# Optimization experiments

Measured on AMD Instinct MI355X. Metric: run time of the kernel, lower is better.

Reference implementation:

```python
import jax, jax.numpy as jnp
import numpy as np

N_PATCHES = 7
HIDDEN = 256
HEADS = 8
BLOCKS = 4
OUT_D = 1000
BATCH = 256
C, H_IMG, W_IMG = 3, 224, 224
N_TOK = N_PATCHES ** 2 + 1  # 50 (CLS at node 0)
INPUT_D = C * (H_IMG // N_PATCHES) * (W_IMG // N_PATCHES)  # 3072
MLP_D = 4 * HIDDEN


def build_edge_index():
    # replicates get_squere_edge_index: 8-neighborhood grid (nodes shifted +1)
    # plus patch->CLS edges. Row 0 = source, row 1 = target (PyG convention).
    s, d = [], []
    for i in range(N_PATCHES):
        for j in range(N_PATCHES):
            a = i + j * N_PATCHES + 1
            for di, dj in [(-1, 0), (-1, -1), (0, -1), (1, -1), (1, 0), (1, 1), (0, 1), (-1, 1)]:
                ii, jj = i + di, j + dj
                if 0 <= ii < N_PATCHES and 0 <= jj < N_PATCHES:
                    s.append(a); d.append(ii + jj * N_PATCHES + 1)
    for i in range(N_PATCHES):
        for j in range(N_PATCHES):
            s.append(i + j * N_PATCHES + 1); d.append(0)
    return np.array([s, d], dtype=np.int64)


def pos_emb(S, d):
    i = jnp.arange(S, dtype=jnp.float32)[:, None]
    j = jnp.arange(d)
    jeff = (j // 2 * 2).astype(jnp.float32)
    ang = i / jnp.power(jnp.float32(10000.0), jeff / d)
    return jnp.where(j % 2 == 0, jnp.sin(ang), jnp.cos(ang))


def layer_norm(x, g, b):
    mu = x.mean(-1, keepdims=True)
    var = ((x - mu) ** 2).mean(-1, keepdims=True)
    return (x - mu) / jnp.sqrt(var + 1e-5) * g + b


def gat(x, src, dst, W, a_s, a_d, bias):
    # PyG GATConv: lin (no bias), per-head additive attention, LeakyReLU(0.2),
    # softmax over incoming edges per target, concat heads, + bias.
    B, N, _ = x.shape
    H, Dh = a_s.shape
    h = (x @ W).reshape(B, N, H, Dh)
    al_s = jnp.einsum('bnhd,hd->bnh', h, a_s)
    al_d = jnp.einsum('bnhd,hd->bnh', h, a_d)
    e = jax.nn.leaky_relu(al_s[:, src] + al_d[:, dst], 0.2)  # [B,E,H]
    seg_max = jax.vmap(lambda v: jax.ops.segment_max(v, dst, num_segments=N))
    seg_sum = jax.vmap(lambda v: jax.ops.segment_sum(v, dst, num_segments=N))
    m = jax.lax.stop_gradient(seg_max(e))
    ex = jnp.exp(e - m[:, dst])
    alpha = ex / (seg_sum(ex)[:, dst] + 1e-16)
    out = seg_sum(h[:, src] * alpha[..., None])  # [B,N,H,Dh]
    return out.reshape(B, N, H * Dh) + bias


def setup_inputs() -> dict:
    key = jax.random.key(0)
    ks = jax.random.split(key, 16)
    sc = 0.05
    L = BLOCKS
    inp = {
        'images': jax.random.normal(ks[0], (BATCH, C, H_IMG, W_IMG), jnp.float32),
        'edge_index': jnp.asarray(build_edge_index()),
        'Wmap': jax.random.normal(ks[1], (INPUT_D, HIDDEN), jnp.float32) * sc,
        'bmap': jax.random.normal(ks[2], (HIDDEN,), jnp.float32) * sc,
        'cls_tok': jax.random.uniform(ks[3], (1, HIDDEN), jnp.float32),
        'Wgat': jax.random.normal(ks[4], (L, HIDDEN, HIDDEN), jnp.float32) * sc,
        'att_src': jax.random.normal(ks[5], (L, HEADS, HIDDEN // HEADS), jnp.float32) * sc,
        'att_dst': jax.random.normal(ks[6], (L, HEADS, HIDDEN // HEADS), jnp.float32) * sc,
        'bgat': jax.random.normal(ks[7], (L, HIDDEN), jnp.float32) * sc,
        'ln1_g': jnp.ones((L, HIDDEN), jnp.float32),
        'ln1_b': jnp.zeros((L, HIDDEN), jnp.float32),
        'ln2_g': jnp.ones((L, HIDDEN), jnp.float32),
        'ln2_b': jnp.zeros((L, HIDDEN), jnp.float32),
        'W1': jax.random.normal(ks[8], (L, HIDDEN, MLP_D), jnp.float32) * sc,
        'b1': jax.random.normal(ks[9], (L, MLP_D), jnp.float32) * sc,
        'W2': jax.random.normal(ks[10], (L, MLP_D, HIDDEN), jnp.float32) * sc,
        'b2': jax.random.normal(ks[11], (L, HIDDEN), jnp.float32) * sc,
        'Wout': jax.random.normal(ks[12], (HIDDEN, OUT_D), jnp.float32) * sc,
        'bout': jax.random.normal(ks[13], (OUT_D,), jnp.float32) * sc,
    }
    return inp


def reference(images, edge_index, Wmap, bmap, cls_tok, Wgat, att_src, att_dst, bgat,
              ln1_g, ln1_b, ln2_g, ln2_b, W1, b1, W2, b2, Wout, bout):
    n, c, h, w = images.shape
    ps = h // N_PATCHES
    # vectorized patchify: [n, np^2, c*ps*ps] in (c, hh, ww) flatten order
    patches = images.reshape(n, c, N_PATCHES, ps, N_PATCHES, ps)
    patches = patches.transpose(0, 2, 4, 1, 3, 5).reshape(n, N_PATCHES ** 2, c * ps * ps)
    tok = patches @ Wmap + bmap
    tok = jnp.concatenate([jnp.broadcast_to(cls_tok, (n, 1, HIDDEN)), tok], axis=1)
    out = tok + pos_emb(N_TOK, HIDDEN)
    loops = jnp.arange(N_TOK)  # GATConv add_self_loops
    src = jnp.concatenate([edge_index[0], loops])
    dst = jnp.concatenate([edge_index[1], loops])
    for l in range(BLOCKS):
        out = out + gat(layer_norm(out, ln1_g[l], ln1_b[l]), src, dst,
                        Wgat[l], att_src[l], att_dst[l], bgat[l])
        h2 = layer_norm(out, ln2_g[l], ln2_b[l])
        out = out + (jax.nn.gelu(h2 @ W1[l] + b1[l], approximate=False) @ W2[l] + b2[l])
    return jax.nn.softmax(out[:, 0] @ Wout + bout, axis=-1)
```

## Files before the change

### kernel.cpp

```cpp
#include <hip/hip_runtime.h>
#include <hip/hip_bf16.h>

#define BATCH   256
#define NTOK    50
#define NPATCH  49
#define HID     256
#define HEADS   8
#define DH      32
#define NBLK    4
#define MLPD    1024
#define OUTD    1000
#define KPATCH  3072
#define MROWS   (BATCH*NTOK)
#define MPATCH  (BATCH*NPATCH)
#define MAXDEG  12

typedef __attribute__((ext_vector_type(4))) float  floatx4;
typedef __attribute__((ext_vector_type(8))) __bf16 bf16x8;
typedef __attribute__((ext_vector_type(4))) int    int4v;
typedef __attribute__((ext_vector_type(4))) short  short4v;

__device__ __forceinline__ bool tag_is_bf16(const unsigned short* tag) {
    return tag[0] == 0x3F80u;
}
__device__ __forceinline__ float ldf(const void* p, long i, bool bf) {
    return bf ? __bfloat162float(((const __hip_bfloat16*)p)[i])
              : ((const float*)p)[i];
}
__device__ __forceinline__ short bf16s(float x) {
    __hip_bfloat16 h = __float2bfloat16(x);
    return *(short*)&h;
}

__device__ __forceinline__ float fast_gelu(float u) {
    float s  = u * 0.70710678118654752f;
    float ax = fabsf(s);
    float t  = 1.f / (1.f + 0.3275911f * ax);
    float p  = fmaf(1.061405429f, t, -1.453152027f);
    p = fmaf(p, t, 1.421413741f);
    p = fmaf(p, t, -0.284496736f);
    p = fmaf(p, t, 0.254829592f);
    p *= t;
    float er = copysignf(1.f - p * __expf(-s * s), s);
    return 0.5f * u * (1.f + er);
}

#define OFF_BMAP 0
#define OFF_CLS  256
#define OFF_ASRC 512
#define OFF_ADST 1536
#define OFF_BGAT 2560
#define OFF_LN1G 3584
#define OFF_LN1B 4608
#define OFF_LN2G 5632
#define OFF_LN2B 6656
#define OFF_B1   7680
#define OFF_B2   11776
#define OFF_BOUT 12800
#define SP_TOTAL 13800

struct SmallSrc {
    const void *bmap, *cls, *asrc, *adst, *bgat, *ln1g, *ln1b, *ln2g, *ln2b, *b1, *b2, *bout;
};

__global__ void pack_params(SmallSrc s, const unsigned short* tag,
                            __hip_bfloat16* __restrict__ sp) {
    bool bf = tag_is_bf16(tag);
    int idx = blockIdx.x * 256 + threadIdx.x;
    if (idx >= SP_TOTAL) return;
    const void* src; long off;
    if      (idx < OFF_CLS)  { src = s.bmap; off = idx; }
    else if (idx < OFF_ASRC) { src = s.cls;  off = idx - OFF_CLS; }
    else if (idx < OFF_ADST) { src = s.asrc; off = idx - OFF_ASRC; }
    else if (idx < OFF_BGAT) { src = s.adst; off = idx - OFF_ADST; }
    else if (idx < OFF_LN1G) { src = s.bgat; off = idx - OFF_BGAT; }
    else if (idx < OFF_LN1B) { src = s.ln1g; off = idx - OFF_LN1G; }
    else if (idx < OFF_LN2G) { src = s.ln1b; off = idx - OFF_LN1B; }
    else if (idx < OFF_LN2B) { src = s.ln2g; off = idx - OFF_LN2G; }
    else if (idx < OFF_B1)   { src = s.ln2b; off = idx - OFF_LN2B; }
    else if (idx < OFF_B2)   { src = s.b1;   off = idx - OFF_B1; }
    else if (idx < OFF_BOUT) { src = s.b2;   off = idx - OFF_B2; }
    else                     { src = s.bout; off = idx - OFF_BOUT; }
    sp[idx] = __float2bfloat16(ldf(src, off, bf));
}

__global__ void prep_kernel(const int* __restrict__ ei, int E0,
                            float* __restrict__ adj, float* __restrict__ pe,
                            int* __restrict__ nbrI, float* __restrict__ nbrW,
                            int* __restrict__ deg) {
    int tid = threadIdx.x;
    if (blockIdx.x == 0) {
        for (int i = tid; i < NTOK * NTOK; i += 64) adj[i] = 0.f;
        __syncthreads();
        bool is64 = (ei[1] == 0);
        for (int e = tid; e < E0; e += 64) {
            int s, d;
            if (is64) { s = ei[2 * e]; d = ei[2 * (E0 + e)]; }
            else      { s = ei[e];     d = ei[E0 + e]; }
            if ((unsigned)s < NTOK && (unsigned)d < NTOK)
                atomicAdd(&adj[d * NTOK + s], 1.f);
        }
        if (tid < NTOK) atomicAdd(&adj[tid * NTOK + tid], 1.f);
        __syncthreads();
        if (tid > 0 && tid < NTOK) {
            int d = 0;
            for (int s = 0; s < NTOK; ++s) {
                float c = adj[tid * NTOK + s];
                if (c > 0.f && d < MAXDEG) { nbrI[tid * MAXDEG + d] = s;
                                             nbrW[tid * MAXDEG + d] = c; ++d; }
            }
            deg[tid] = d;
        }
        if (tid == 0) deg[0] = 0;
    } else {
        int t = blockIdx.x - 1;
        for (int j = tid; j < HID; j += 64) {
            float jeff = (float)(j & ~1);
            float ang = (float)t / powf(10000.f, jeff / (float)HID);
            pe[t * HID + j] = ((j & 1) == 0) ? sinf(ang) : cosf(ang);
        }
    }
}

__global__ __launch_bounds__(256) void transpose2(
    const void* __restrict__ Wmap, const void* __restrict__ Wgat,
    const void* __restrict__ W1,   const void* __restrict__ W2,
    const void* __restrict__ Wout, const unsigned short* tag,
    __hip_bfloat16* __restrict__ wmapT, __hip_bfloat16* __restrict__ wgatT,
    __hip_bfloat16* __restrict__ w1T,   __hip_bfloat16* __restrict__ w2T,
    __hip_bfloat16* __restrict__ woutT) {
    __shared__ __hip_bfloat16 tl[64][65];
    bool bf = tag_is_bf16(tag);
    int b = blockIdx.x;
    const void* src; __hip_bfloat16* dst; int R, C, tR; long so, dofs;
    if (b < 192)      { src = Wmap; dst = wmapT; R = 3072; C = 256;  tR = 48;
                        so = 0; dofs = 0; }
    else if (b < 256) { int ti = b - 192, l = ti >> 4; b = ti & 15;
                        src = Wgat; dst = wgatT; R = 256; C = 256; tR = 4;
                        so = (long)l * 65536; dofs = so; goto tiled; }
    else if (b < 512) { int ti = b - 256, l = ti >> 6; b = ti & 63;
                        src = W1; dst = w1T; R = 256; C = 1024; tR = 4;
                        so = (long)l * 262144; dofs = so; goto tiled; }
    else if (b < 768) { int ti = b - 512, l = ti >> 6; b = ti & 63;
                        src = W2; dst = w2T; R = 1024; C = 256; tR = 16;
                        so = (long)l * 262144; dofs = so; goto tiled; }
    else              { b -= 768; src = Wout; dst = woutT; R = 256; C = 1000;
                        tR = 4; so = 0; dofs = 0; }
tiled:
    int r0 = (b % tR) * 64, c0 = (b / tR) * 64;
    int tx = threadIdx.x & 63, ty = threadIdx.x >> 6;
#pragma unroll
    for (int j = 0; j < 16; ++j) {
        int rr = ty + 4 * j;
        float v = (c0 + tx < C) ? ldf(src, so + (long)(r0 + rr) * C + c0 + tx, bf) : 0.f;
        tl[rr][tx] = __float2bfloat16(v);
    }
    __syncthreads();
#pragma unroll
    for (int j = 0; j < 16; ++j) {
        int i2 = ty + 4 * j;
        if (c0 + i2 < C)
            dst[dofs + (long)(c0 + i2) * R + r0 + tx] = tl[tx][i2];
    }
}

__global__ void init_resid(const __hip_bfloat16* __restrict__ sp,
                           const float* __restrict__ pe, float* __restrict__ resid) {
    int idx = blockIdx.x * 256 + threadIdx.x;
    int row = idx >> 6, c4 = (idx & 63) * 4, t = row % NTOK;
    floatx4 o;
#pragma unroll
    for (int i = 0; i < 4; ++i) {
        int c = c4 + i;
        o[i] = (t == 0) ? __bfloat162float(sp[OFF_CLS + c]) + pe[c]
                        : __bfloat162float(sp[OFF_BMAP + c]) + pe[t * HID + c];
    }
    ((floatx4*)resid)[idx] = o;
}

__global__ __launch_bounds__(256) void patch_gemm64(
    const void* __restrict__ img, const __hip_bfloat16* __restrict__ wmapT,
    const unsigned short* tag, float* __restrict__ resid) {
    __shared__ short As[2][64][32];
    __shared__ short Bs[2][64][32];
    bool bf = tag_is_bf16(tag);
    int tid = threadIdx.x;
    int L = blockIdx.x;
    int w = (L & 7) * 98 + (L >> 3);
    int m0 = (w >> 2) * 64, n0 = (w & 3) * 64;
    int lr = tid >> 2, lc = (tid & 3) * 8;
    int lane = tid & 63, wave = tid >> 6;
    int wm = (wave >> 1) * 32, wn = (wave & 1) * 32;
    int q = lane >> 4, r = lane & 15, q8 = q * 8;
    int mA = m0 + lr;
    long baseA;
    { int pb = mA / 49, pp = mA % 49; baseA = (long)pb * 150528 + (pp / 7) * 7168 + (pp % 7) * 32; }
    const short* Bg = (const short*)wmapT;
    long b0 = (long)(n0 + lr) * KPATCH + lc;
    floatx4 acc[2][2];
#pragma unroll
    for (int i = 0; i < 2; ++i)
#pragma unroll
        for (int j = 0; j < 2; ++j) acc[i][j] = floatx4{0.f, 0.f, 0.f, 0.f};
    floatx4 f0_0, f1_0, f0_1, f1_1;
    bf16x8  h_0, h_1;
    int4v   bv_0, bv_1;
    auto loadA = [&](int ku, floatx4& f0, floatx4& f1, bf16x8& h) {
        long g = baseA + (ku >> 5) * 50176 + (ku & 31) * 224 + lc;
        if (bf) { h = *(const bf16x8*)(((const __bf16*)img) + g); }
        else    { const float* f = (const float*)img;
                  f0 = *(const floatx4*)(f + g);
                  f1 = *(const floatx4*)(f + g + 4); }
    };
    auto cvtA = [&](const floatx4& f0, const floatx4& f1, const bf16x8& h) -> bf16x8 {
        if (bf) return h;
        union { bf16x8 v; __hip_bfloat16 hh[8]; } u;
#pragma unroll
        for (int j = 0; j < 4; ++j) { u.hh[j]     = __float2bfloat16(f0[j]);
                                      u.hh[4 + j] = __float2bfloat16(f1[j]); }
        return u.v;
    };
    loadA(0, f0_0, f1_0, h_0); bv_0 = *(const int4v*)(Bg + b0);
    loadA(1, f0_1, f1_1, h_1); bv_1 = *(const int4v*)(Bg + b0 + 32);
    *(bf16x8*)&As[0][lr][lc] = cvtA(f0_0, f1_0, h_0);
    *(int4v*)&Bs[0][lr][lc]  = bv_0;
    loadA(2, f0_0, f1_0, h_0); bv_0 = *(const int4v*)(Bg + b0 + 64);
    __syncthreads();
    for (int kt = 0; kt < 96; kt += 2) {
        {
            *(bf16x8*)&As[1][lr][lc] = cvtA(f0_1, f1_1, h_1);
            *(int4v*)&Bs[1][lr][lc]  = bv_1;
            if (kt + 3 < 96) {
                loadA(kt + 3, f0_1, f1_1, h_1);
                bv_1 = *(const int4v*)(Bg + b0 + (long)(kt + 3) * 32);
            }
            bf16x8 af[2], bfv[2];
#pragma unroll
            for (int i = 0; i < 2; ++i) af[i]  = *(const bf16x8*)&As[0][wm + 16 * i + r][q8];
#pragma unroll
            for (int j = 0; j < 2; ++j) bfv[j] = *(const bf16x8*)&Bs[0][wn + 16 * j + r][q8];
#pragma unroll
            for (int i = 0; i < 2; ++i)
#pragma unroll
                for (int j = 0; j < 2; ++j)
                    acc[i][j] = __builtin_amdgcn_mfma_f32_16x16x32_bf16(af[i], bfv[j], acc[i][j], 0, 0, 0);
            __syncthreads();
        }
        {
            if (kt + 2 < 96) {
                *(bf16x8*)&As[0][lr][lc] = cvtA(f0_0, f1_0, h_0);
                *(int4v*)&Bs[0][lr][lc]  = bv_0;
                if (kt + 4 < 96) {
                    loadA(kt + 4, f0_0, f1_0, h_0);
                    bv_0 = *(const int4v*)(Bg + b0 + (long)(kt + 4) * 32);
                }
            }
            bf16x8 af[2], bfv[2];
#pragma unroll
            for (int i = 0; i < 2; ++i) af[i]  = *(const bf16x8*)&As[1][wm + 16 * i + r][q8];
#pragma unroll
            for (int j = 0; j < 2; ++j) bfv[j] = *(const bf16x8*)&Bs[1][wn + 16 * j + r][q8];
#pragma unroll
            for (int i = 0; i < 2; ++i)
#pragma unroll
                for (int j = 0; j < 2; ++j)
                    acc[i][j] = __builtin_amdgcn_mfma_f32_16x16x32_bf16(af[i], bfv[j], acc[i][j], 0, 0, 0);
            __syncthreads();
        }
    }
#pragma unroll
    for (int j = 0; j < 2; ++j) {
        int col = n0 + wn + 16 * j + r;
#pragma unroll
        for (int i = 0; i < 2; ++i) {
#pragma unroll
            for (int reg = 0; reg < 4; ++reg) {
                int row = m0 + wm + 16 * i + q * 4 + reg;
                int bb = row / 49, pp = row % 49;
                long oi = ((long)bb * NTOK + pp + 1) * HID + col;
                resid[oi] += acc[i][j][reg];
            }
        }
    }
}

__global__ __launch_bounds__(512) void fused_layers(
    float* __restrict__ resid, const __hip_bfloat16* __restrict__ sp,
    const __hip_bfloat16* __restrict__ wgatT, const __hip_bfloat16* __restrict__ w1T,
    const __hip_bfloat16* __restrict__ w2T,
    const float* __restrict__ adj, const int* __restrict__ nbrI,
    const float* __restrict__ nbrW, const int* __restrict__ deg) {
    __shared__ __align__(16) char smem[141392];
    float (*resS)[HID]  = (float (*)[HID])(smem);
    short (*xbS)[264]   = (short (*)[264])(smem + 51200);
    float (*hS)[HID]    = (float (*)[HID])(smem + 84992);
    short (*midS)[264]  = (short (*)[264])(smem + 84992);
    float (*als)[HEADS] = (float (*)[HEADS])(smem + 51200);
    float (*ald)[HEADS] = (float (*)[HEADS])(smem + 52800);
    float (*alpha0)[NTOK] = (float (*)[NTOK])(smem + 54400);
    float (*alphaC)[NTOK][MAXDEG] = (float (*)[NTOK][MAXDEG])(smem + 56000);
    float* attS = (float*)(smem + 75200);
    float* attD = (float*)(smem + 76224);
    float* bgv  = (float*)(smem + 77248);
    int   (*nIs)[MAXDEG] = (int (*)[MAXDEG])(smem + 136192);
    float (*nWs)[MAXDEG] = (float (*)[MAXDEG])(smem + 138592);
    int*   dgs  = (int*)(smem + 140992);
    float* adj0 = (float*)(smem + 141192);

    int b = blockIdx.x, tid = threadIdx.x;
    int wave = tid >> 6, lane = tid & 63;
    int q = lane >> 4, r = lane & 15, q8 = q * 8;
    int nq = wave * 32;

    float* rg = resid + (long)b * (NTOK * HID);
    for (int i = tid; i < NTOK * HID / 4; i += 512)
        ((floatx4*)resS)[i] = ((const floatx4*)rg)[i];
    for (int i = tid; i < 14 * 132; i += 512) ((int*)&xbS[50][0])[i] = 0;
    for (int i = tid; i < NTOK * MAXDEG; i += 512) {
        ((int*)nIs)[i] = nbrI[i];
        ((float*)nWs)[i] = nbrW[i];
    }
    if (tid < NTOK) { dgs[tid] = deg[tid]; adj0[tid] = adj[tid]; }
    __syncthreads();

    for (int l = 0; l < NBLK; ++l) {
        {
            const __hip_bfloat16* gp = sp + OFF_LN1G + l * HID;
            const __hip_bfloat16* bp = sp + OFF_LN1B + l * HID;
            float gv[4], bvv[4];
#pragma unroll
            for (int u = 0; u < 4; ++u) { gv[u]  = __bfloat162float(gp[lane + 64 * u]);
                                          bvv[u] = __bfloat162float(bp[lane + 64 * u]); }
            for (int row = wave; row < NTOK; row += 8) {
                float v[4];
#pragma unroll
                for (int u = 0; u < 4; ++u) v[u] = resS[row][lane + 64 * u];
                float s = v[0] + v[1] + v[2] + v[3];
#pragma unroll
                for (int off = 32; off; off >>= 1) s += __shfl_xor(s, off, 64);
                float mu = s * (1.f / HID), d2 = 0.f;
#pragma unroll
                for (int u = 0; u < 4; ++u) { float d = v[u] - mu; d2 += d * d; }
#pragma unroll
                for (int off = 32; off; off >>= 1) d2 += __shfl_xor(d2, off, 64);
                float rstd = rsqrtf(d2 * (1.f / HID) + 1e-5f);
#pragma unroll
                for (int u = 0; u < 4; ++u)
                    xbS[row][lane + 64 * u] = bf16s((v[u] - mu) * rstd * gv[u] + bvv[u]);
            }
        }
        __syncthreads();
        {
            const short* Bg = (const short*)wgatT + (long)l * HID * HID;
            bf16x8 af[4][8];
#pragma unroll
            for (int i = 0; i < 4; ++i)
#pragma unroll
                for (int kk = 0; kk < 8; ++kk)
                    af[i][kk] = *(const bf16x8*)&xbS[16 * i + r][kk * 32 + q8];
            floatx4 acc[4][2];
#pragma unroll
            for (int i = 0; i < 4; ++i)
#pragma unroll
                for (int j = 0; j < 2; ++j) acc[i][j] = floatx4{0.f, 0.f, 0.f, 0.f};
#pragma unroll
            for (int j = 0; j < 2; ++j) {
                const short* Bp = Bg + (long)(nq + 16 * j + r) * HID + q8;
                bf16x8 bv[8];
#pragma unroll
                for (int kk = 0; kk < 8; ++kk) bv[kk] = *(const bf16x8*)(Bp + kk * 32);
#pragma unroll
                for (int kk = 0; kk < 8; ++kk)
#pragma unroll
                    for (int i = 0; i < 4; ++i)
                        acc[i][j] = __builtin_amdgcn_mfma_f32_16x16x32_bf16(af[i][kk], bv[kk], acc[i][j], 0, 0, 0);
            }
#pragma unroll
            for (int j = 0; j < 2; ++j) {
                int col = nq + 16 * j + r;
#pragma unroll
                for (int i = 0; i < 4; ++i)
#pragma unroll
                    for (int reg = 0; reg < 4; ++reg) {
                        int row = 16 * i + q * 4 + reg;
                        if (row < NTOK) hS[row][col] = acc[i][j][reg];
                    }
            }
        }
        __syncthreads();
        if (tid < HID) {
            attS[tid] = __bfloat162float(sp[OFF_ASRC + l * HID + tid]);
            attD[tid] = __bfloat162float(sp[OFF_ADST + l * HID + tid]);
            bgv[tid]  = __bfloat162float(sp[OFF_BGAT + l * HID + tid]);
        }
        __syncthreads();
        if (tid < NTOK * HEADS) {
            int s = tid >> 3, hh = tid & 7;
            float a1 = 0.f, a2 = 0.f;
#pragma unroll
            for (int d = 0; d < DH; ++d) {
                float hv = hS[s][hh * DH + d];
                a1 += hv * attS[hh * DH + d];
                a2 += hv * attD[hh * DH + d];
            }
            als[s][hh] = a1; ald[s][hh] = a2;
        }
        __syncthreads();
        if (tid < NTOK * HEADS) {
            int t = tid >> 3, hh = tid & 7;
            float aldt = ald[t][hh];
            if (t == 0) {
                float mx = -1e30f;
                for (int s = 0; s < NTOK; ++s) {
                    float w = adj0[s];
                    if (w > 0.f) {
                        float e = als[s][hh] + aldt; e = (e > 0.f) ? e : 0.2f * e;
                        mx = fmaxf(mx, e);
                    }
                }
                float sum = 0.f;
                for (int s = 0; s < NTOK; ++s) {
                    float w = adj0[s], v = 0.f;
                    if (w > 0.f) {
                        float e = als[s][hh] + aldt; e = (e > 0.f) ? e : 0.2f * e;
                        v = w * expf(e - mx);
                    }
                    alpha0[hh][s] = v; sum += v;
                }
                float inv = 1.f / (sum + 1e-16f);
                for (int s = 0; s < NTOK; ++s) alpha0[hh][s] *= inv;
            } else {
                int d = dgs[t];
                float mx = -1e30f;
                for (int j = 0; j < d; ++j) {
                    float e = als[nIs[t][j]][hh] + aldt; e = (e > 0.f) ? e : 0.2f * e;
                    mx = fmaxf(mx, e);
                }
                float sum = 0.f;
                for (int j = 0; j < d; ++j) {
                    float e = als[nIs[t][j]][hh] + aldt; e = (e > 0.f) ? e : 0.2f * e;
                    float w = nWs[t][j] * expf(e - mx);
                    alphaC[hh][t][j] = w; sum += w;
                }
                float inv = 1.f / (sum + 1e-16f);
                for (int j = 0; j < d; ++j) alphaC[hh][t][j] *= inv;
            }
        }
        __syncthreads();
        {
            int half = tid >> 8;
            int col = tid & 255;
            int hd = col >> 5;
            float bgc = bgv[col];
            for (int t = half; t < NTOK; t += 2) {
                float a = 0.f;
                if (t == 0) {
                    for (int s = 0; s < NTOK; ++s) a += alpha0[hd][s] * hS[s][col];
                } else {
                    int d = dgs[t];
                    for (int j = 0; j < d; ++j) a += alphaC[hd][t][j] * hS[nIs[t][j]][col];
                }
                resS[t][col] += a + bgc;
            }
        }
        __syncthreads();
        {
            const __hip_bfloat16* gp = sp + OFF_LN2G + l * HID;
            const __hip_bfloat16* bp = sp + OFF_LN2B + l * HID;
            float gv[4], bvv[4];
#pragma unroll
            for (int u = 0; u < 4; ++u) { gv[u]  = __bfloat162float(gp[lane + 64 * u]);
                                          bvv[u] = __bfloat162float(bp[lane + 64 * u]); }
            for (int row = wave; row < NTOK; row += 8) {
                float v[4];
#pragma unroll
                for (int u = 0; u < 4; ++u) v[u] = resS[row][lane + 64 * u];
                float s = v[0] + v[1] + v[2] + v[3];
#pragma unroll
                for (int off = 32; off; off >>= 1) s += __shfl_xor(s, off, 64);
                float mu = s * (1.f / HID), d2 = 0.f;
#pragma unroll
                for (int u = 0; u < 4; ++u) { float d = v[u] - mu; d2 += d * d; }
#pragma unroll
                for (int off = 32; off; off >>= 1) d2 += __shfl_xor(d2, off, 64);
                float rstd = rsqrtf(d2 * (1.f / HID) + 1e-5f);
#pragma unroll
                for (int u = 0; u < 4; ++u)
                    xbS[row][lane + 64 * u] = bf16s((v[u] - mu) * rstd * gv[u] + bvv[u]);
            }
            for (int i = tid; i < 14 * 132; i += 512) ((int*)&xbS[50][0])[i] = 0;
        }
        __syncthreads();
        {
            const short* Bg1 = (const short*)w1T + (long)l * HID * MLPD;
            const short* Bg2 = (const short*)w2T + (long)l * HID * MLPD;
            floatx4 acc2[4][2];
#pragma unroll
            for (int i = 0; i < 4; ++i)
#pragma unroll
                for (int j = 0; j < 2; ++j) acc2[i][j] = floatx4{0.f, 0.f, 0.f, 0.f};
            for (int c = 0; c < 4; ++c) {
                {
                    bf16x8 af[4][8];
#pragma unroll
                    for (int i = 0; i < 4; ++i)
#pragma unroll
                        for (int kk = 0; kk < 8; ++kk)
                            af[i][kk] = *(const bf16x8*)&xbS[16 * i + r][kk * 32 + q8];
                    floatx4 accm[4][2];
#pragma unroll
                    for (int i = 0; i < 4; ++i)
#pragma unroll
                        for (int j = 0; j < 2; ++j) accm[i][j] = floatx4{0.f, 0.f, 0.f, 0.f};
#pragma unroll
                    for (int j = 0; j < 2; ++j) {
                        const short* Bp = Bg1 + (long)(c * 256 + nq + 16 * j + r) * HID + q8;
                        bf16x8 bv[8];
#pragma unroll
                        for (int kk = 0; kk < 8; ++kk) bv[kk] = *(const bf16x8*)(Bp + kk * 32);
#pragma unroll
                        for (int kk = 0; kk < 8; ++kk)
#pragma unroll
                            for (int i = 0; i < 4; ++i)
                                accm[i][j] = __builtin_amdgcn_mfma_f32_16x16x32_bf16(af[i][kk], bv[kk], accm[i][j], 0, 0, 0);
                    }
#pragma unroll
                    for (int j = 0; j < 2; ++j) {
                        int colL = nq + 16 * j + r;
                        float b1v = __bfloat162float(sp[OFF_B1 + l * MLPD + c * 256 + colL]);
#pragma unroll
                        for (int i = 0; i < 4; ++i)
#pragma unroll
                            for (int reg = 0; reg < 4; ++reg) {
                                int row = 16 * i + q * 4 + reg;
                                midS[row][colL] = bf16s(fast_gelu(accm[i][j][reg] + b1v));
                            }
                    }
                }
                __syncthreads();
                {
                    bf16x8 af2[4][8];
#pragma unroll
                    for (int i = 0; i < 4; ++i)
#pragma unroll
                        for (int kk = 0; kk < 8; ++kk)
                            af2[i][kk] = *(const bf16x8*)&midS[16 * i + r][kk * 32 + q8];
#pragma unroll
                    for (int j = 0; j < 2; ++j) {
                        const short* Bp = Bg2 + (long)(nq + 16 * j + r) * MLPD + c * 256 + q8;
                        bf16x8 bv[8];
#pragma unroll
                        for (int kk = 0; kk < 8; ++kk) bv[kk] = *(const bf16x8*)(Bp + kk * 32);
#pragma unroll
                        for (int kk = 0; kk < 8; ++kk)
#pragma unroll
                            for (int i = 0; i < 4; ++i)
                                acc2[i][j] = __builtin_amdgcn_mfma_f32_16x16x32_bf16(af2[i][kk], bv[kk], acc2[i][j], 0, 0, 0);
                    }
                }
                __syncthreads();
            }
#pragma unroll
            for (int j = 0; j < 2; ++j) {
                int col = nq + 16 * j + r;
                float b2v = __bfloat162float(sp[OFF_B2 + l * HID + col]);
#pragma unroll
                for (int i = 0; i < 4; ++i)
#pragma unroll
                    for (int reg = 0; reg < 4; ++reg) {
                        int row = 16 * i + q * 4 + reg;
                        if (row < NTOK) resS[row][col] += acc2[i][j][reg] + b2v;
                    }
            }
        }
        __syncthreads();
    }
    for (int i = tid; i < NTOK * HID / 4; i += 512)
        ((floatx4*)rg)[i] = ((const floatx4*)resS)[i];
}

__global__ __launch_bounds__(256) void head_gemm(
    const float* __restrict__ resid, const __hip_bfloat16* __restrict__ BT,
    const __hip_bfloat16* __restrict__ bias, float* __restrict__ logits, int N) {
    __shared__ short As[64][32];
    __shared__ short Bs[64][32];
    int tid = threadIdx.x;
    int m0 = blockIdx.x * 64, n0 = blockIdx.y * 64;
    int lr = tid >> 2, lc = (tid & 3) * 8;
    int lane = tid & 63, wave = tid >> 6;
    int wm = (wave >> 1) * 32, wn = (wave & 1) * 32;
    int q = lane >> 4, r = lane & 15, q8 = q * 8;
    const short* Bg = (const short*)BT;
    long a0 = (long)(m0 + lr) * (NTOK * HID) + lc;
    int bn = n0 + lr;
    long b0 = (long)bn * HID + lc;
    bool v0 = bn < N;
    floatx4 acc[2][2];
#pragma unroll
    for (int i = 0; i < 2; ++i)
#pragma unroll
        for (int j = 0; j < 2; ++j) acc[i][j] = floatx4{0.f, 0.f, 0.f, 0.f};
    int4v za = {0, 0, 0, 0};
    auto loadA = [&](int k0) -> bf16x8 {
        floatx4 f0 = *(const floatx4*)(resid + a0 + k0);
        floatx4 f1 = *(const floatx4*)(resid + a0 + k0 + 4);
        union { bf16x8 v; __hip_bfloat16 h[8]; } u;
#pragma unroll
        for (int i = 0; i < 4; ++i) { u.h[i] = __float2bfloat16(f0[i]);
                                      u.h[4 + i] = __float2bfloat16(f1[i]); }
        return u.v;
    };
    bf16x8 av = loadA(0);
    int4v bv = v0 ? *(const int4v*)(Bg + b0) : za;
    for (int kt = 0; kt < 8; ++kt) {
        __syncthreads();
        *(bf16x8*)&As[lr][lc] = av;
        *(int4v*)&Bs[lr][lc] = bv;
        __syncthreads();
        if (kt < 7) {
            av = loadA((kt + 1) * 32);
            bv = v0 ? *(const int4v*)(Bg + b0 + (kt + 1) * 32) : za;
        }
        bf16x8 af[2], bfv[2];
#pragma unroll
        for (int i = 0; i < 2; ++i) af[i]  = *(const bf16x8*)&As[wm + 16 * i + r][q8];
#pragma unroll
        for (int j = 0; j < 2; ++j) bfv[j] = *(const bf16x8*)&Bs[wn + 16 * j + r][q8];
#pragma unroll
        for (int i = 0; i < 2; ++i)
#pragma unroll
            for (int j = 0; j < 2; ++j)
                acc[i][j] = __builtin_amdgcn_mfma_f32_16x16x32_bf16(af[i], bfv[j], acc[i][j], 0, 0, 0);
    }
#pragma unroll
    for (int j = 0; j < 2; ++j) {
        int col = n0 + wn + 16 * j + r;
        if (col >= N) continue;
        float bvv = __bfloat162float(bias[col]);
#pragma unroll
        for (int i = 0; i < 2; ++i)
#pragma unroll
            for (int reg = 0; reg < 4; ++reg) {
                int row = m0 + wm + 16 * i + q * 4 + reg;
                logits[(long)row * N + col] = acc[i][j][reg] + bvv;
            }
    }
}

__global__ __launch_bounds__(256) void softmax_kernel(
    const float* __restrict__ logits, const unsigned short* tag, void* __restrict__ out) {
    __shared__ float red[8];
    bool bf = tag_is_bf16(tag);
    int b = blockIdx.x, tid = threadIdx.x;
    const float* Lr = logits + (long)b * OUTD;
    float v[4], mx = -1e30f;
#pragma unroll
    for (int i = 0; i < 4; ++i) {
        int j = tid + i * 256;
        v[i] = (j < OUTD) ? Lr[j] : -1e30f;
        mx = fmaxf(mx, v[i]);
    }
#pragma unroll
    for (int off = 32; off; off >>= 1) mx = fmaxf(mx, __shfl_xor(mx, off, 64));
    if ((tid & 63) == 0) red[tid >> 6] = mx;
    __syncthreads();
    mx = fmaxf(fmaxf(red[0], red[1]), fmaxf(red[2], red[3]));
    float s = 0.f, ex[4];
#pragma unroll
    for (int i = 0; i < 4; ++i) {
        int j = tid + i * 256;
        ex[i] = (j < OUTD) ? expf(v[i] - mx) : 0.f;
        s += ex[i];
    }
#pragma unroll
    for (int off = 32; off; off >>= 1) s += __shfl_xor(s, off, 64);
    __syncthreads();
    if ((tid & 63) == 0) red[4 + (tid >> 6)] = s;
    __syncthreads();
    float inv = 1.f / (red[4] + red[5] + red[6] + red[7]);
#pragma unroll
    for (int i = 0; i < 4; ++i) {
        int j = tid + i * 256;
        if (j < OUTD) {
            float o = ex[i] * inv;
            if (bf) ((__hip_bfloat16*)out)[(long)b * OUTD + j] = __float2bfloat16(o);
            else    ((float*)out)[(long)b * OUTD + j] = o;
        }
    }
}

extern "C" void kernel_launch(void* const* d_in, const int* in_sizes, int n_in,
                              void* d_out, int out_size, void* d_ws, size_t ws_size,
                              hipStream_t stream) {
    const void* images = d_in[0];
    const int*  ei     = (const int*)d_in[1];
    const unsigned short* tag = (const unsigned short*)d_in[9];
    int E0 = in_sizes[1] / 2;

    char* p = (char*)d_ws;
    auto alloc = [&](size_t bytes) { char* r = p; p += (bytes + 255) & ~(size_t)255; return r; };
    float*          resid  = (float*)alloc((size_t)MROWS * HID * 4);
    float*          logits = (float*)alloc((size_t)BATCH * OUTD * 4);
    float*          pe     = (float*)alloc((size_t)NTOK * HID * 4);
    float*          adj    = (float*)alloc((size_t)NTOK * NTOK * 4);
    int*            nbrI   = (int*)alloc((size_t)NTOK * MAXDEG * 4);
    float*          nbrW   = (float*)alloc((size_t)NTOK * MAXDEG * 4);
    int*            degp   = (int*)alloc((size_t)NTOK * 4);
    __hip_bfloat16* smallp = (__hip_bfloat16*)alloc((size_t)SP_TOTAL * 2);
    __hip_bfloat16* wmapT  = (__hip_bfloat16*)alloc((size_t)KPATCH * HID * 2);
    __hip_bfloat16* wgatT  = (__hip_bfloat16*)alloc((size_t)NBLK * HID * HID * 2);
    __hip_bfloat16* w1T    = (__hip_bfloat16*)alloc((size_t)NBLK * HID * MLPD * 2);
    __hip_bfloat16* w2T    = (__hip_bfloat16*)alloc((size_t)NBLK * HID * MLPD * 2);
    __hip_bfloat16* woutT  = (__hip_bfloat16*)alloc((size_t)HID * OUTD * 2);

    SmallSrc ss = { d_in[3], d_in[4], d_in[6], d_in[7], d_in[8], d_in[9], d_in[10],
                    d_in[11], d_in[12], d_in[14], d_in[16], d_in[18] };
    prep_kernel<<<51, 64, 0, stream>>>(ei, E0, adj, pe, nbrI, nbrW, degp);
    pack_params<<<(SP_TOTAL + 255) / 256, 256, 0, stream>>>(ss, tag, smallp);
    transpose2<<<832, 256, 0, stream>>>(d_in[2], d_in[5], d_in[13], d_in[15],
                                        d_in[17], tag, wmapT, wgatT, w1T, w2T, woutT);
    init_resid<<<MROWS * HID / 1024, 256, 0, stream>>>(smallp, pe, resid);
    patch_gemm64<<<784, 256, 0, stream>>>(images, wmapT, tag, resid);

    fused_layers<<<BATCH, 512, 0, stream>>>(resid, smallp, wgatT, w1T, w2T,
                                            adj, nbrI, nbrW, degp);

    head_gemm<<<dim3(BATCH / 64, (OUTD + 63) / 64), 256, 0, stream>>>(
        resid, woutT, smallp + OFF_BOUT, logits, OUTD);
    softmax_kernel<<<BATCH, 256, 0, stream>>>(logits, tag, d_out);
}
```

Measured before the change: 725.6 us.

## Double fused_layers block to 1024 threads, halve per-wave GEMM column tile

The fused per-sample transformer kernel now launches 1024 threads (16 waves) instead of 512. Each wave computes 16 output columns instead of 32 and reads A fragments from LDS inside the MFMA loop instead of preloading them into registers. The CLS-node softmax moves from one serial thread per head to a wave-wide shuffle reduction, while the other waves handle the patch nodes in parallel. This aims to raise wave-level parallelism per CU and cut register pressure, at the cost of more LDS traffic for A fragments and heavier barriers. With about 141KB of LDS per block, only one block fits per CU either way.

```diff
diff --git a/kernel.cpp b/kernel.cpp
--- a/kernel.cpp
+++ b/kernel.cpp
@@ -284,7 +284,7 @@
     }
 }
 
-__global__ __launch_bounds__(512) void fused_layers(
+__global__ __launch_bounds__(1024) void fused_layers(
     float* __restrict__ resid, const __hip_bfloat16* __restrict__ sp,
     const __hip_bfloat16* __restrict__ wgatT, const __hip_bfloat16* __restrict__ w1T,
     const __hip_bfloat16* __restrict__ w2T,
@@ -310,15 +310,15 @@
     int b = blockIdx.x, tid = threadIdx.x;
     int wave = tid >> 6, lane = tid & 63;
     int q = lane >> 4, r = lane & 15, q8 = q * 8;
-    int nq = wave * 32;
+    int nq = wave * 16;
 
     float* rg = resid + (long)b * (NTOK * HID);
-    for (int i = tid; i < NTOK * HID / 4; i += 512)
+    for (int i = tid; i < NTOK * HID / 4; i += 1024)
         ((floatx4*)resS)[i] = ((const floatx4*)rg)[i];
-    for (int i = tid; i < 14 * 132; i += 512) ((int*)&xbS[50][0])[i] = 0;
-    for (int i = tid; i < NTOK * MAXDEG; i += 512) {
-        ((int*)nIs)[i] = nbrI[i];
-        ((float*)nWs)[i] = nbrW[i];
+    for (int i = tid; i < 14 * 132; i += 1024) ((int*)&xbS[50][0])[i] = 0;
+    if (tid < NTOK * MAXDEG) {
+        ((int*)nIs)[tid] = nbrI[tid];
+        ((float*)nWs)[tid] = nbrW[tid];
     }
     if (tid < NTOK) { dgs[tid] = deg[tid]; adj0[tid] = adj[tid]; }
     __syncthreads();
@@ -331,7 +331,7 @@
 #pragma unroll
             for (int u = 0; u < 4; ++u) { gv[u]  = __bfloat162float(gp[lane + 64 * u]);
                                           bvv[u] = __bfloat162float(bp[lane + 64 * u]); }
-            for (int row = wave; row < NTOK; row += 8) {
+            for (int row = wave; row < NTOK; row += 16) {
                 float v[4];
 #pragma unroll
                 for (int u = 0; u < 4; ++u) v[u] = resS[row][lane + 64 * u];
@@ -352,40 +352,29 @@
         __syncthreads();
         {
             const short* Bg = (const short*)wgatT + (long)l * HID * HID;
-            bf16x8 af[4][8];
+            const short* Bp = Bg + (long)(nq + r) * HID + q8;
+            bf16x8 bv[8];
+#pragma unroll
+            for (int kk = 0; kk < 8; ++kk) bv[kk] = *(const bf16x8*)(Bp + kk * 32);
+            floatx4 acc[4];
+#pragma unroll
+            for (int i = 0; i < 4; ++i) acc[i] = floatx4{0.f, 0.f, 0.f, 0.f};
+#pragma unroll
+            for (int kk = 0; kk < 8; ++kk) {
+#pragma unroll
+                for (int i = 0; i < 4; ++i) {
+                    bf16x8 af = *(const bf16x8*)&xbS[16 * i + r][kk * 32 + q8];
+                    acc[i] = __builtin_amdgcn_mfma_f32_16x16x32_bf16(af, bv[kk], acc[i], 0, 0, 0);
+                }
+            }
+            int col = nq + r;
 #pragma unroll
             for (int i = 0; i < 4; ++i)
 #pragma unroll
-                for (int kk = 0; kk < 8; ++kk)
-                    af[i][kk] = *(const bf16x8*)&xbS[16 * i + r][kk * 32 + q8];
-            floatx4 acc[4][2];
-#pragma unroll
-            for (int i = 0; i < 4; ++i)
-#pragma unroll
-                for (int j = 0; j < 2; ++j) acc[i][j] = floatx4{0.f, 0.f, 0.f, 0.f};
-#pragma unroll
-            for (int j = 0; j < 2; ++j) {
-                const short* Bp = Bg + (long)(nq + 16 * j + r) * HID + q8;
-                bf16x8 bv[8];
-#pragma unroll
-                for (int kk = 0; kk < 8; ++kk) bv[kk] = *(const bf16x8*)(Bp + kk * 32);
-#pragma unroll
-                for (int kk = 0; kk < 8; ++kk)
-#pragma unroll
-                    for (int i = 0; i < 4; ++i)
-                        acc[i][j] = __builtin_amdgcn_mfma_f32_16x16x32_bf16(af[i][kk], bv[kk], acc[i][j], 0, 0, 0);
-            }
-#pragma unroll
-            for (int j = 0; j < 2; ++j) {
-                int col = nq + 16 * j + r;
-#pragma unroll
-                for (int i = 0; i < 4; ++i)
-#pragma unroll
-                    for (int reg = 0; reg < 4; ++reg) {
-                        int row = 16 * i + q * 4 + reg;
-                        if (row < NTOK) hS[row][col] = acc[i][j][reg];
-                    }
-            }
+                for (int reg = 0; reg < 4; ++reg) {
+                    int row = 16 * i + q * 4 + reg;
+                    if (row < NTOK) hS[row][col] = acc[i][reg];
+                }
         }
         __syncthreads();
         if (tid < HID) {
@@ -406,30 +395,31 @@
             als[s][hh] = a1; ald[s][hh] = a2;
         }
         __syncthreads();
-        if (tid < NTOK * HEADS) {
-            int t = tid >> 3, hh = tid & 7;
-            float aldt = ald[t][hh];
-            if (t == 0) {
-                float mx = -1e30f;
-                for (int s = 0; s < NTOK; ++s) {
-                    float w = adj0[s];
-                    if (w > 0.f) {
-                        float e = als[s][hh] + aldt; e = (e > 0.f) ? e : 0.2f * e;
-                        mx = fmaxf(mx, e);
-                    }
-                }
-                float sum = 0.f;
-                for (int s = 0; s < NTOK; ++s) {
-                    float w = adj0[s], v = 0.f;
-                    if (w > 0.f) {
-                        float e = als[s][hh] + aldt; e = (e > 0.f) ? e : 0.2f * e;
-                        v = w * expf(e - mx);
-                    }
-                    alpha0[hh][s] = v; sum += v;
-                }
-                float inv = 1.f / (sum + 1e-16f);
-                for (int s = 0; s < NTOK; ++s) alpha0[hh][s] *= inv;
-            } else {
+        if (tid < 512) {
+            int hh = wave;
+            int s = lane;
+            float w = 0.f, e = -1e30f;
+            if (s < NTOK) {
+                w = adj0[s];
+                if (w > 0.f) {
+                    e = als[s][hh] + ald[0][hh];
+                    e = (e > 0.f) ? e : 0.2f * e;
+                }
+            }
+            float mx = e;
+#pragma unroll
+            for (int off = 32; off; off >>= 1) mx = fmaxf(mx, __shfl_xor(mx, off, 64));
+            float v = (s < NTOK && w > 0.f) ? w * expf(e - mx) : 0.f;
+            float sum = v;
+#pragma unroll
+            for (int off = 32; off; off >>= 1) sum += __shfl_xor(sum, off, 64);
+            float inv = 1.f / (sum + 1e-16f);
+            if (s < NTOK) alpha0[hh][s] = v * inv;
+        } else {
+            int t2 = tid - 512;
+            if (t2 < NPATCH * HEADS) {
+                int t = (t2 >> 3) + 1, hh = t2 & 7;
+                float aldt = ald[t][hh];
                 int d = dgs[t];
                 float mx = -1e30f;
                 for (int j = 0; j < d; ++j) {
@@ -448,11 +438,11 @@
         }
         __syncthreads();
         {
-            int half = tid >> 8;
+            int quarter = tid >> 8;
             int col = tid & 255;
             int hd = col >> 5;
             float bgc = bgv[col];
-            for (int t = half; t < NTOK; t += 2) {
+            for (int t = quarter; t < NTOK; t += 4) {
                 float a = 0.f;
                 if (t == 0) {
                     for (int s = 0; s < NTOK; ++s) a += alpha0[hd][s] * hS[s][col];
@@ -471,7 +461,7 @@
 #pragma unroll
             for (int u = 0; u < 4; ++u) { gv[u]  = __bfloat162float(gp[lane + 64 * u]);
                                           bvv[u] = __bfloat162float(bp[lane + 64 * u]); }
-            for (int row = wave; row < NTOK; row += 8) {
+            for (int row = wave; row < NTOK; row += 16) {
                 float v[4];
 #pragma unroll
                 for (int u = 0; u < 4; ++u) v[u] = resS[row][lane + 64 * u];
@@ -488,94 +478,72 @@
                 for (int u = 0; u < 4; ++u)
                     xbS[row][lane + 64 * u] = bf16s((v[u] - mu) * rstd * gv[u] + bvv[u]);
             }
-            for (int i = tid; i < 14 * 132; i += 512) ((int*)&xbS[50][0])[i] = 0;
+            for (int i = tid; i < 14 * 132; i += 1024) ((int*)&xbS[50][0])[i] = 0;
         }
         __syncthreads();
         {
             const short* Bg1 = (const short*)w1T + (long)l * HID * MLPD;
             const short* Bg2 = (const short*)w2T + (long)l * HID * MLPD;
-            floatx4 acc2[4][2];
-#pragma unroll
-            for (int i = 0; i < 4; ++i)
-#pragma unroll
-                for (int j = 0; j < 2; ++j) acc2[i][j] = floatx4{0.f, 0.f, 0.f, 0.f};
+            floatx4 acc2[4];
+#pragma unroll
+            for (int i = 0; i < 4; ++i) acc2[i] = floatx4{0.f, 0.f, 0.f, 0.f};
             for (int c = 0; c < 4; ++c) {
                 {
-                    bf16x8 af[4][8];
+                    const short* Bp = Bg1 + (long)(c * 256 + nq + r) * HID + q8;
+                    bf16x8 bv[8];
+#pragma unroll
+                    for (int kk = 0; kk < 8; ++kk) bv[kk] = *(const bf16x8*)(Bp + kk * 32);
+                    floatx4 accm[4];
+#pragma unroll
+                    for (int i = 0; i < 4; ++i) accm[i] = floatx4{0.f, 0.f, 0.f, 0.f};
+#pragma unroll
+                    for (int kk = 0; kk < 8; ++kk) {
+#pragma unroll
+                        for (int i = 0; i < 4; ++i) {
+                            bf16x8 af = *(const bf16x8*)&xbS[16 * i + r][kk * 32 + q8];
+                            accm[i] = __builtin_amdgcn_mfma_f32_16x16x32_bf16(af, bv[kk], accm[i], 0, 0, 0);
+                        }
+                    }
+                    int colL = nq + r;
+                    float b1v = __bfloat162float(sp[OFF_B1 + l * MLPD + c * 256 + colL]);
 #pragma unroll
                     for (int i = 0; i < 4; ++i)
 #pragma unroll
-                        for (int kk = 0; kk < 8; ++kk)
-                            af[i][kk] = *(const bf16x8*)&xbS[16 * i + r][kk * 32 + q8];
-                    floatx4 accm[4][2];
-#pragma unroll
-                    for (int i = 0; i < 4; ++i)
-#pragma unroll
-                        for (int j = 0; j < 2; ++j) accm[i][j] = floatx4{0.f, 0.f, 0.f, 0.f};
-#pragma unroll
-                    for (int j = 0; j < 2; ++j) {
-                        const short* Bp = Bg1 + (long)(c * 256 + nq + 16 * j + r) * HID + q8;
-                        bf16x8 bv[8];
-#pragma unroll
-                        for (int kk = 0; kk < 8; ++kk) bv[kk] = *(const bf16x8*)(Bp + kk * 32);
-#pragma unroll
-                        for (int kk = 0; kk < 8; ++kk)
-#pragma unroll
-                            for (int i = 0; i < 4; ++i)
-                                accm[i][j] = __builtin_amdgcn_mfma_f32_16x16x32_bf16(af[i][kk], bv[kk], accm[i][j], 0, 0, 0);
-                    }
-#pragma unroll
-                    for (int j = 0; j < 2; ++j) {
-                        int colL = nq + 16 * j + r;
-                        float b1v = __bfloat162float(sp[OFF_B1 + l * MLPD + c * 256 + colL]);
-#pragma unroll
-                        for (int i = 0; i < 4; ++i)
-#pragma unroll
-                            for (int reg = 0; reg < 4; ++reg) {
-                                int row = 16 * i + q * 4 + reg;
-                                midS[row][colL] = bf16s(fast_gelu(accm[i][j][reg] + b1v));
-                            }
-                    }
+                        for (int reg = 0; reg < 4; ++reg) {
+                            int row = 16 * i + q * 4 + reg;
+                            midS[row][colL] = bf16s(fast_gelu(accm[i][reg] + b1v));
+                        }
                 }
                 __syncthreads();
                 {
-                    bf16x8 af2[4][8];
-#pragma unroll
-                    for (int i = 0; i < 4; ++i)
-#pragma unroll
-                        for (int kk = 0; kk < 8; ++kk)
-                            af2[i][kk] = *(const bf16x8*)&midS[16 * i + r][kk * 32 + q8];
-#pragma unroll
-                    for (int j = 0; j < 2; ++j) {
-                        const short* Bp = Bg2 + (long)(nq + 16 * j + r) * MLPD + c * 256 + q8;
-                        bf16x8 bv[8];
-#pragma unroll
-                        for (int kk = 0; kk < 8; ++kk) bv[kk] = *(const bf16x8*)(Bp + kk * 32);
-#pragma unroll
-                        for (int kk = 0; kk < 8; ++kk)
-#pragma unroll
-                            for (int i = 0; i < 4; ++i)
-                                acc2[i][j] = __builtin_amdgcn_mfma_f32_16x16x32_bf16(af2[i][kk], bv[kk], acc2[i][j], 0, 0, 0);
+                    const short* Bp = Bg2 + (long)(nq + r) * MLPD + c * 256 + q8;
+                    bf16x8 bv[8];
+#pragma unroll
+                    for (int kk = 0; kk < 8; ++kk) bv[kk] = *(const bf16x8*)(Bp + kk * 32);
+#pragma unroll
+                    for (int kk = 0; kk < 8; ++kk) {
+#pragma unroll
+                        for (int i = 0; i < 4; ++i) {
+                            bf16x8 af = *(const bf16x8*)&midS[16 * i + r][kk * 32 + q8];
+                            acc2[i] = __builtin_amdgcn_mfma_f32_16x16x32_bf16(af, bv[kk], acc2[i], 0, 0, 0);
+                        }
                     }
                 }
                 __syncthreads();
             }
-#pragma unroll
-            for (int j = 0; j < 2; ++j) {
-                int col = nq + 16 * j + r;
-                float b2v = __bfloat162float(sp[OFF_B2 + l * HID + col]);
-#pragma unroll
-                for (int i = 0; i < 4; ++i)
-#pragma unroll
-                    for (int reg = 0; reg < 4; ++reg) {
-                        int row = 16 * i + q * 4 + reg;
-                        if (row < NTOK) resS[row][col] += acc2[i][j][reg] + b2v;
-                    }
-            }
-        }
-        __syncthreads();
-    }
-    for (int i = tid; i < NTOK * HID / 4; i += 512)
+            int col = nq + r;
+            float b2v = __bfloat162float(sp[OFF_B2 + l * HID + col]);
+#pragma unroll
+            for (int i = 0; i < 4; ++i)
+#pragma unroll
+                for (int reg = 0; reg < 4; ++reg) {
+                    int row = 16 * i + q * 4 + reg;
+                    if (row < NTOK) resS[row][col] += acc2[i][reg] + b2v;
+                }
+        }
+        __syncthreads();
+    }
+    for (int i = tid; i < NTOK * HID / 4; i += 1024)
         ((floatx4*)rg)[i] = ((const floatx4*)resS)[i];
 }
 
@@ -722,8 +690,8 @@
     init_resid<<<MROWS * HID / 1024, 256, 0, stream>>>(smallp, pe, resid);
     patch_gemm64<<<784, 256, 0, stream>>>(images, wmapT, tag, resid);
 
-    fused_layers<<<BATCH, 512, 0, stream>>>(resid, smallp, wgatT, w1T, w2T,
-                                            adj, nbrI, nbrW, degp);
+    fused_layers<<<BATCH, 1024, 0, stream>>>(resid, smallp, wgatT, w1T, w2T,
+                                             adj, nbrI, nbrW, degp);
 
     head_gemm<<<dim3(BATCH / 64, (OUTD + 63) / 64), 256, 0, stream>>>(
         resid, woutT, smallp + OFF_BOUT, logits, OUTD);
```

Measured after the change: 629.3 us. 13.3% less time.
